# Kernel tuning notes

Hardware: AMD Instinct MI355X
Metric: run time of the kernel (lower is better)

## Reference

```python
import jax, jax.numpy as jnp
import numpy as np

VOL_SIZE = 1.0  # config.render.volume_size


def _make_grid(G, vol_size):
    # pytorch3d Volumes.get_coord_grid(world_coordinates=True): axis-aligned grid
    # centered at origin, spacing = voxel_size = vol_size/G, last dim is (x,y,z)
    # with x varying along W, y along H, z along D.
    m = (G - 1) / 2.0 * (vol_size / G)
    lin = jnp.linspace(-m, m, G, dtype=jnp.float32)
    zz, yy, xx = jnp.meshgrid(lin, lin, lin, indexing='ij')
    return jnp.stack([xx, yy, zz], axis=-1)  # [G,G,G,3]


def _grid_sample_3d(vol, grid):
    # vol: [N,C,D,H,W]; grid: [N,Dg,Hg,Wg,3] xyz in [-1,1].
    # Matches torch F.grid_sample(mode='bilinear', padding_mode='zeros', align_corners=False).
    N, C, D, H, W = vol.shape
    ix = ((grid[..., 0] + 1.0) * W - 1.0) * 0.5
    iy = ((grid[..., 1] + 1.0) * H - 1.0) * 0.5
    iz = ((grid[..., 2] + 1.0) * D - 1.0) * 0.5
    x0f, y0f, z0f = jnp.floor(ix), jnp.floor(iy), jnp.floor(iz)
    tx, ty, tz = ix - x0f, iy - y0f, iz - z0f
    x0, y0, z0 = x0f.astype(jnp.int32), y0f.astype(jnp.int32), z0f.astype(jnp.int32)

    def per_batch(v, z0, y0, x0, tx, ty, tz):
        # v: [C,D,H,W]; index/weight maps: [Dg,Hg,Wg]
        def corner(z, y, x):
            valid = (z >= 0) & (z < D) & (y >= 0) & (y < H) & (x >= 0) & (x < W)
            zc = jnp.clip(z, 0, D - 1)
            yc = jnp.clip(y, 0, H - 1)
            xc = jnp.clip(x, 0, W - 1)
            return v[:, zc, yc, xc] * valid[None]  # [C,Dg,Hg,Wg]
        z1, y1, x1 = z0 + 1, y0 + 1, x0 + 1
        acc = jnp.zeros((C,) + z0.shape, dtype=v.dtype)
        for zc, wz in ((z0, 1.0 - tz), (z1, tz)):
            for yc, wy in ((y0, 1.0 - ty), (y1, ty)):
                for xc, wx in ((x0, 1.0 - tx), (x1, tx)):
                    acc = acc + corner(zc, yc, xc) * (wz * wy * wx)[None]
        return acc

    return jax.vmap(per_batch)(vol, z0, y0, x0, tx, ty, tz)


def reference(voxels, camPoses_cv2, grid_size):
    B, t, C, D, H, W = voxels.shape
    G = grid_size
    m = (G - 1) / 2.0 * (VOL_SIZE / G)  # grid_coord_max
    grid_coord = _make_grid(G, VOL_SIZE)  # [G,G,G,3]

    # T = pose_0 @ pose_1^{-1}, per (B, t-1) pair
    pose0 = jnp.broadcast_to(camPoses_cv2[:, 0:1], (B, t - 1, 4, 4)).reshape(B * (t - 1), 4, 4)
    pose1 = camPoses_cv2[:, 1:].reshape(B * (t - 1), 4, 4)
    T = pose0 @ jnp.linalg.inv(pose1)

    # homogeneous transform of world grid points: cam = R @ p + trans
    pts = grid_coord.reshape(-1, 3)  # [N=G^3, 3]
    R, trans = T[:, :3, :3], T[:, :3, 3]
    cam = jnp.einsum('nij,pj->npi', R, pts) + trans[:, None, :]  # [B*(t-1), N, 3]
    sample_grid = (cam / m).reshape(B * (t - 1), D, H, W, 3)

    warped = _grid_sample_3d(voxels[:, 1:].reshape(B * (t - 1), C, D, H, W), sample_grid)
    out = jnp.concatenate([voxels[:, 0:1], warped.reshape(B, t - 1, C, D, H, W)], axis=1)
    return out


def setup_inputs() -> dict:
    key = jax.random.key(0)
    kv, ka, kt = jax.random.split(key, 3)
    B, t, C, G = 2, 5, 16, 64
    voxels = jax.random.normal(kv, (B, t, C, G, G, G), dtype=jnp.float32)
    # build valid SE(3)-ish camera poses (orthonormal rotation + small translation)
    A = jax.random.normal(ka, (B, t, 3, 3), dtype=jnp.float32)
    Q, _ = jnp.linalg.qr(A)
    det = jnp.linalg.det(Q)
    Q = Q * jnp.sign(det)[..., None, None]  # ensure det=+1
    trans = 0.2 * jax.random.normal(kt, (B, t, 3), dtype=jnp.float32)
    top = jnp.concatenate([Q, trans[..., None]], axis=-1)  # [B,t,3,4]
    bottom = jnp.broadcast_to(jnp.array([0.0, 0.0, 0.0, 1.0], jnp.float32), (B, t, 1, 4))
    camPoses_cv2 = jnp.concatenate([top, bottom], axis=-2)  # [B,t,4,4]
    return {"voxels": voxels, "camPoses_cv2": camPoses_cv2, "grid_size": G}
```

## Files before the change

### kernel.cpp

```cpp
#include <hip/hip_runtime.h>

#define G3_    (64 * 64 * 64)
#define CCH    16
#define TT     5
#define LSTRIDE 17
#define BUF    4096
#define NCHB   4
#define NWARP  (4096 * (CCH / NCHB))
#define NCOPY  8192
#define NBLK   (NWARP + NCOPY)


__global__ void coeff_kernel(const float* __restrict__ cam, float* __restrict__ Tc)
{
    int n = threadIdx.x;
    if (n >= 8) return;
    int b = n >> 2, j = n & 3;
    const float* p0 = cam + (size_t)(b * TT) * 16;
    const float* p1 = cam + (size_t)(b * TT + j + 1) * 16;
    float a00 = p0[0], a01 = p0[1], a02 = p0[2],  at0 = p0[3];
    float a10 = p0[4], a11 = p0[5], a12 = p0[6],  at1 = p0[7];
    float a20 = p0[8], a21 = p0[9], a22 = p0[10], at2 = p0[11];
    float b00 = p1[0], b01 = p1[1], b02 = p1[2],  bt0 = p1[3];
    float b10 = p1[4], b11 = p1[5], b12 = p1[6],  bt1 = p1[7];
    float b20 = p1[8], b21 = p1[9], b22 = p1[10], bt2 = p1[11];
    float R00 = a00*b00 + a01*b01 + a02*b02;
    float R01 = a00*b10 + a01*b11 + a02*b12;
    float R02 = a00*b20 + a01*b21 + a02*b22;
    float R10 = a10*b00 + a11*b01 + a12*b02;
    float R11 = a10*b10 + a11*b11 + a12*b12;
    float R12 = a10*b20 + a11*b21 + a12*b22;
    float R20 = a20*b00 + a21*b01 + a22*b02;
    float R21 = a20*b10 + a21*b11 + a22*b12;
    float R22 = a20*b20 + a21*b21 + a22*b22;
    float trx = at0 - (R00*bt0 + R01*bt1 + R02*bt2);
    float try_= at1 - (R10*bt0 + R11*bt1 + R12*bt2);
    float trz = at2 - (R20*bt0 + R21*bt1 + R22*bt2);

    const float S  = 1.0f / 64.0f;
    const float SC = 32.0f / 0.4921875f;
    float ax = SC * R00 * S, bx = SC * R01 * S, cx = SC * R02 * S;
    float ay = SC * R10 * S, by = SC * R11 * S, cy = SC * R12 * S;
    float az = SC * R20 * S, bz = SC * R21 * S, cz = SC * R22 * S;
    float* o = Tc + n * 12;
    o[0] = ax; o[1] = bx; o[2] = cx;
    o[3] = ay; o[4] = by; o[5] = cy;
    o[6] = az; o[7] = bz; o[8] = cz;
    o[9]  = -31.5f * (ax + bx + cx) + SC * trx + 31.5f;
    o[10] = -31.5f * (ay + by + cy) + SC * try_ + 31.5f;
    o[11] = -31.5f * (az + bz + cz) + SC * trz + 31.5f;
}

__global__ __launch_bounds__(256) void fused_kernel(const float* __restrict__ vox,
                                                    const float* __restrict__ Tc,
                                                    float* __restrict__ out)
{
    __shared__ float lds[BUF];
    const int tid = threadIdx.x;

    const int bid  = blockIdx.x;
    const int sbid = (bid & 7) * (NBLK / 8) + (bid >> 3);
    const int q3   = sbid / 3;
    const int r3   = sbid - q3 * 3;

    if (r3 == 2) {
        int t4 = q3 * 256 + tid;
        int b  = t4 >> 20;
        int rr = t4 & ((1 << 20) - 1);
        size_t base = (size_t)(b * TT) * CCH * G3_;
        const float4* s = (const float4*)(vox + base);
        float4* d = (float4*)(out + base);
        d[rr] = s[rr];
        return;
    }

    const int wid = q3 * 2 + r3;
    const int cg  = wid >> 12;
    const int t9  = wid & 4095;
    const int n   = t9 >> 9;
    const int t6  = t9 & 511;
    const int ox  = (t6 & 7) << 3;
    const int oy  = ((t6 >> 3) & 7) << 3;
    const int oz  = (t6 >> 6) << 3;
    const int b   = n >> 2, j = n & 3;

    const float* Cp = Tc + n * 12;
    const float ax = Cp[0], bx = Cp[1], cx = Cp[2];
    const float ay = Cp[3], by = Cp[4], cy = Cp[5];
    const float az = Cp[6], bz = Cp[7], cz = Cp[8];
    const float kx = Cp[9], ky = Cp[10], kz = Cp[11];

    float x0a = ax * ox, x0b = ax * (ox + 7);
    float x1a = bx * oy, x1b = bx * (oy + 7);
    float x2a = cx * oz, x2b = cx * (oz + 7);
    float min_ix = kx + fminf(x0a, x0b) + fminf(x1a, x1b) + fminf(x2a, x2b);
    float max_ix = kx + fmaxf(x0a, x0b) + fmaxf(x1a, x1b) + fmaxf(x2a, x2b);
    float y0a = ay * ox, y0b = ay * (ox + 7);
    float y1a = by * oy, y1b = by * (oy + 7);
    float y2a = cy * oz, y2b = cy * (oz + 7);
    float min_iy = ky + fminf(y0a, y0b) + fminf(y1a, y1b) + fminf(y2a, y2b);
    float max_iy = ky + fmaxf(y0a, y0b) + fmaxf(y1a, y1b) + fmaxf(y2a, y2b);
    float z0a = az * ox, z0b = az * (ox + 7);
    float z1a = bz * oy, z1b = bz * (oy + 7);
    float z2a = cz * oz, z2b = cz * (oz + 7);
    float min_iz = kz + fminf(z0a, z0b) + fminf(z1a, z1b) + fminf(z2a, z2b);
    float max_iz = kz + fmaxf(z0a, z0b) + fmaxf(z1a, z1b) + fmaxf(z2a, z2b);

    int xlo = min(max((int)floorf(min_ix), 0), 63);
    int xhi = min(max((int)floorf(max_ix) + 1, 0), 63);
    int ylo = min(max((int)floorf(min_iy), 0), 63);
    int yhi = min(max((int)floorf(max_iy) + 1, 0), 63);
    int zlo = min(max((int)floorf(min_iz), 0), 63);
    int zhi = min(max((int)floorf(max_iz) + 1, 0), 63);
    const int xlo_e = xlo & ~1;
    const int sxe = xhi - xlo_e + 1;
    const int sy  = yhi - ylo + 1;
    const int sz  = zhi - zlo + 1;
    const int lstep = sy * LSTRIDE;

    const int gx0 = ox + ((tid & 3) << 1);
    const int gy  = oy + ((tid >> 2) & 7);
    const int gz  = oz + (tid >> 5);
    const float ix0 = kx + ax * gx0 + bx * gy + cx * gz;
    const float iy0 = ky + ay * gx0 + by * gy + cy * gz;
    const float iz0 = kz + az * gx0 + bz * gy + cz * gz;

    float wx0[2], wx1[2], wy0[2], wy1[2], wz0[2], wz1[2];
    int base0[2], base1[2];
    #pragma unroll
    for (int k = 0; k < 2; ++k) {
        float ix = ix0 + (k ? ax : 0.0f);
        float iy = iy0 + (k ? ay : 0.0f);
        float iz = iz0 + (k ? az : 0.0f);
        float fx = floorf(ix), fy = floorf(iy), fz = floorf(iz);
        float tx = ix - fx, ty = iy - fy, tz = iz - fz;
        int X0 = (int)fx, Y0 = (int)fy, Z0 = (int)fz;

        float w0 = ((unsigned)X0 < 64u) ? (1.0f - tx) : 0.0f;
        float w1 = ((unsigned)(X0 + 1) < 64u) ? tx : 0.0f;
        int rxu = X0 - xlo_e;
        wx0[k] = (rxu < 0) ? w1 : w0;
        wx1[k] = (rxu < 0) ? 0.0f : w1;
        int rx0 = min(max(rxu, 0), sxe - 1);

        w0 = ((unsigned)Y0 < 64u) ? (1.0f - ty) : 0.0f;
        w1 = ((unsigned)(Y0 + 1) < 64u) ? ty : 0.0f;
        int ryu = Y0 - ylo;
        wy0[k] = (ryu < 0) ? w1 : w0;
        wy1[k] = (ryu < 0) ? 0.0f : w1;
        int ry0 = min(max(ryu, 0), sy - 1);

        wz0[k] = ((unsigned)Z0 < 64u) ? (1.0f - tz) : 0.0f;
        wz1[k] = ((unsigned)(Z0 + 1) < 64u) ? tz : 0.0f;
        int rz0 = min(max(Z0     - zlo, 0), sz - 1);
        int rz1 = min(max(Z0 + 1 - zlo, 0), sz - 1);

        base0[k] = rz0 * lstep + ry0 * LSTRIDE + rx0;
        base1[k] = rz1 * lstep + ry0 * LSTRIDE + rx0;
    }
    const int soff = (gz << 12) + (gy << 6) + gx0;

    const size_t fb = ((size_t)(b * TT + j + 1) * CCH + cg * NCHB) * G3_;
    const float* vbase = vox + fb;
    float* obase = out + fb;

    const int lane8 = tid & 7;
    const int row16 = (tid >> 3) & 15;
    const int zh    = tid >> 7;
    const int xe    = xlo_e + (lane8 << 1);
    const bool actS = (xe <= xhi) && (row16 < sy);
    const int grow  = (zlo << 12) + ((ylo + row16) << 6) + xe;
    const int lrow  = row16 * LSTRIDE + (lane8 << 1);

    float2 stg[8];

    if (actS) {
        const float2* gp = (const float2*)(vbase + grow);
        #pragma unroll
        for (int k = 0; k < 8; ++k) {
            int zz = (k << 1) + zh;
            if (zz < sz) stg[k] = gp[(size_t)zz << 11];
        }
    }
    #pragma unroll
    for (int i = 0; i < 16; ++i) lds[tid + i * 256] = 0.0f;
    __syncthreads();
    if (actS) {
        #pragma unroll
        for (int k = 0; k < 8; ++k) {
            int zz = (k << 1) + zh;
            if (zz < sz) {
                float* wp = lds + lrow + zz * lstep;
                wp[0] = stg[k].x;
                wp[1] = stg[k].y;
            }
        }
    }
    __syncthreads();

    for (int cc = 0; cc < NCHB; ++cc) {
        const bool pre = (cc + 1 < NCHB);
        if (pre && actS) {
            const float2* gp = (const float2*)(vbase + (size_t)(cc + 1) * G3_ + grow);
            #pragma unroll
            for (int k = 0; k < 8; ++k) {
                int zz = (k << 1) + zh;
                if (zz < sz) stg[k] = gp[(size_t)zz << 11];
            }
        }

        float* op = obase + (size_t)cc * G3_;
        float res[2];
        #pragma unroll
        for (int k = 0; k < 2; ++k) {
            const float* pz0 = lds + base0[k];
            const float* pz1 = lds + base1[k];
            float v000 = pz0[0],  v001 = pz0[1];
            float v010 = pz0[17], v011 = pz0[18];
            float v100 = pz1[0],  v101 = pz1[1];
            float v110 = pz1[17], v111 = pz1[18];
            float t00 = v000 * wx0[k] + v001 * wx1[k];
            float t01 = v010 * wx0[k] + v011 * wx1[k];
            float t10 = v100 * wx0[k] + v101 * wx1[k];
            float t11 = v110 * wx0[k] + v111 * wx1[k];
            float u0  = t00 * wy0[k] + t01 * wy1[k];
            float u1  = t10 * wy0[k] + t11 * wy1[k];
            res[k] = u0 * wz0[k] + u1 * wz1[k];
        }
        *(float2*)(op + soff) = make_float2(res[0], res[1]);

        if (pre) {
            __syncthreads();
            if (actS) {
                #pragma unroll
                for (int k = 0; k < 8; ++k) {
                    int zz = (k << 1) + zh;
                    if (zz < sz) {
                        float* wp = lds + lrow + zz * lstep;
                        wp[0] = stg[k].x;
                        wp[1] = stg[k].y;
                    }
                }
            }
            __syncthreads();
        }
    }
}

extern "C" void kernel_launch(void* const* d_in, const int* in_sizes, int n_in,
                              void* d_out, int out_size, void* d_ws, size_t ws_size,
                              hipStream_t stream)
{
    const float* vox = (const float*)d_in[0];
    const float* cam = (const float*)d_in[1];
    float* out = (float*)d_out;
    float* Tc  = (float*)d_ws;

    hipLaunchKernelGGL(coeff_kernel, dim3(1), dim3(64), 0, stream, cam, Tc);
    hipLaunchKernelGGL(fused_kernel, dim3(NBLK), dim3(256), 0, stream, vox, Tc, out);
}
```

Baseline: 357.5 us.

## Replace LDS-staged brick gather with direct global trilinear gathers per channel

Removes the shared-memory staging of the source bounding box and the 4-channel pipelined loop. Each block now handles one channel and a z-slice of 8 y-rows, and gathers its 8 corners straight from global memory, relying on L2/L1 caching. The copy and warp blocks are interleaved 8:1. This drops the syncs and LDS traffic, but trades them for uncoalesced global gathers and eight global loads per output point.

```diff
diff --git a/kernel.cpp b/kernel.cpp
--- a/kernel.cpp
+++ b/kernel.cpp
@@ -3,10 +3,7 @@
 #define G3_    (64 * 64 * 64)
 #define CCH    16
 #define TT     5
-#define LSTRIDE 17
-#define BUF    4096
-#define NCHB   4
-#define NWARP  (4096 * (CCH / NCHB))
+#define NWARP  65536
 #define NCOPY  8192
 #define NBLK   (NWARP + NCOPY)
 
@@ -55,16 +52,15 @@
                                                     const float* __restrict__ Tc,
                                                     float* __restrict__ out)
 {
-    __shared__ float lds[BUF];
     const int tid = threadIdx.x;
 
     const int bid  = blockIdx.x;
     const int sbid = (bid & 7) * (NBLK / 8) + (bid >> 3);
-    const int q3   = sbid / 3;
-    const int r3   = sbid - q3 * 3;
+    const int q9   = sbid / 9;
+    const int r9   = sbid - q9 * 9;
 
-    if (r3 == 2) {
-        int t4 = q3 * 256 + tid;
+    if (r9 == 8) {
+        int t4 = q9 * 256 + tid;
         int b  = t4 >> 20;
         int rr = t4 & ((1 << 20) - 1);
         size_t base = (size_t)(b * TT) * CCH * G3_;
@@ -74,14 +70,14 @@
         return;
     }
 
-    const int wid = q3 * 2 + r3;
-    const int cg  = wid >> 12;
-    const int t9  = wid & 4095;
-    const int n   = t9 >> 9;
-    const int t6  = t9 & 511;
-    const int ox  = (t6 & 7) << 3;
-    const int oy  = ((t6 >> 3) & 7) << 3;
-    const int oz  = (t6 >> 6) << 3;
+    const int wid = q9 * 8 + r9;
+    const int pc  = wid >> 9;
+    const int rem = wid & 511;
+    const int gz  = rem >> 3;
+    const int gy  = ((rem & 7) << 3) + (tid >> 5);
+    const int gx0 = (tid & 31) << 1;
+    const int n   = pc >> 4;
+    const int c   = pc & 15;
     const int b   = n >> 2, j = n & 3;
 
     const float* Cp = Tc + n * 12;
@@ -90,161 +86,53 @@
     const float az = Cp[6], bz = Cp[7], cz = Cp[8];
     const float kx = Cp[9], ky = Cp[10], kz = Cp[11];
 
-    float x0a = ax * ox, x0b = ax * (ox + 7);
-    float x1a = bx * oy, x1b = bx * (oy + 7);
-    float x2a = cx * oz, x2b = cx * (oz + 7);
-    float min_ix = kx + fminf(x0a, x0b) + fminf(x1a, x1b) + fminf(x2a, x2b);
-    float max_ix = kx + fmaxf(x0a, x0b) + fmaxf(x1a, x1b) + fmaxf(x2a, x2b);
-    float y0a = ay * ox, y0b = ay * (ox + 7);
-    float y1a = by * oy, y1b = by * (oy + 7);
-    float y2a = cy * oz, y2b = cy * (oz + 7);
-    float min_iy = ky + fminf(y0a, y0b) + fminf(y1a, y1b) + fminf(y2a, y2b);
-    float max_iy = ky + fmaxf(y0a, y0b) + fmaxf(y1a, y1b) + fmaxf(y2a, y2b);
-    float z0a = az * ox, z0b = az * (ox + 7);
-    float z1a = bz * oy, z1b = bz * (oy + 7);
-    float z2a = cz * oz, z2b = cz * (oz + 7);
-    float min_iz = kz + fminf(z0a, z0b) + fminf(z1a, z1b) + fminf(z2a, z2b);
-    float max_iz = kz + fmaxf(z0a, z0b) + fmaxf(z1a, z1b) + fmaxf(z2a, z2b);
+    const size_t fb = ((size_t)(b * TT + j + 1) * CCH + c) * G3_;
+    const float* v = vox + fb;
 
-    int xlo = min(max((int)floorf(min_ix), 0), 63);
-    int xhi = min(max((int)floorf(max_ix) + 1, 0), 63);
-    int ylo = min(max((int)floorf(min_iy), 0), 63);
-    int yhi = min(max((int)floorf(max_iy) + 1, 0), 63);
-    int zlo = min(max((int)floorf(min_iz), 0), 63);
-    int zhi = min(max((int)floorf(max_iz) + 1, 0), 63);
-    const int xlo_e = xlo & ~1;
-    const int sxe = xhi - xlo_e + 1;
-    const int sy  = yhi - ylo + 1;
-    const int sz  = zhi - zlo + 1;
-    const int lstep = sy * LSTRIDE;
+    float ix = kx + ax * gx0 + bx * gy + cx * gz;
+    float iy = ky + ay * gx0 + by * gy + cy * gz;
+    float iz = kz + az * gx0 + bz * gy + cz * gz;
 
-    const int gx0 = ox + ((tid & 3) << 1);
-    const int gy  = oy + ((tid >> 2) & 7);
-    const int gz  = oz + (tid >> 5);
-    const float ix0 = kx + ax * gx0 + bx * gy + cx * gz;
-    const float iy0 = ky + ay * gx0 + by * gy + cy * gz;
-    const float iz0 = kz + az * gx0 + bz * gy + cz * gz;
-
-    float wx0[2], wx1[2], wy0[2], wy1[2], wz0[2], wz1[2];
-    int base0[2], base1[2];
+    float res[2];
     #pragma unroll
     for (int k = 0; k < 2; ++k) {
-        float ix = ix0 + (k ? ax : 0.0f);
-        float iy = iy0 + (k ? ay : 0.0f);
-        float iz = iz0 + (k ? az : 0.0f);
+        if (k) { ix += ax; iy += ay; iz += az; }
         float fx = floorf(ix), fy = floorf(iy), fz = floorf(iz);
         float tx = ix - fx, ty = iy - fy, tz = iz - fz;
         int X0 = (int)fx, Y0 = (int)fy, Z0 = (int)fz;
 
-        float w0 = ((unsigned)X0 < 64u) ? (1.0f - tx) : 0.0f;
-        float w1 = ((unsigned)(X0 + 1) < 64u) ? tx : 0.0f;
-        int rxu = X0 - xlo_e;
-        wx0[k] = (rxu < 0) ? w1 : w0;
-        wx1[k] = (rxu < 0) ? 0.0f : w1;
-        int rx0 = min(max(rxu, 0), sxe - 1);
+        float wx0 = ((unsigned)X0       < 64u) ? (1.0f - tx) : 0.0f;
+        float wx1 = ((unsigned)(X0 + 1) < 64u) ? tx          : 0.0f;
+        float wy0 = ((unsigned)Y0       < 64u) ? (1.0f - ty) : 0.0f;
+        float wy1 = ((unsigned)(Y0 + 1) < 64u) ? ty          : 0.0f;
+        float wz0 = ((unsigned)Z0       < 64u) ? (1.0f - tz) : 0.0f;
+        float wz1 = ((unsigned)(Z0 + 1) < 64u) ? tz          : 0.0f;
 
-        w0 = ((unsigned)Y0 < 64u) ? (1.0f - ty) : 0.0f;
-        w1 = ((unsigned)(Y0 + 1) < 64u) ? ty : 0.0f;
-        int ryu = Y0 - ylo;
-        wy0[k] = (ryu < 0) ? w1 : w0;
-        wy1[k] = (ryu < 0) ? 0.0f : w1;
-        int ry0 = min(max(ryu, 0), sy - 1);
+        int xc0 = min(max(X0,     0), 63), xc1 = min(max(X0 + 1, 0), 63);
+        int yc0 = min(max(Y0,     0), 63), yc1 = min(max(Y0 + 1, 0), 63);
+        int zc0 = min(max(Z0,     0), 63), zc1 = min(max(Z0 + 1, 0), 63);
 
-        wz0[k] = ((unsigned)Z0 < 64u) ? (1.0f - tz) : 0.0f;
-        wz1[k] = ((unsigned)(Z0 + 1) < 64u) ? tz : 0.0f;
-        int rz0 = min(max(Z0     - zlo, 0), sz - 1);
-        int rz1 = min(max(Z0 + 1 - zlo, 0), sz - 1);
+        int zy00 = (zc0 << 12) + (yc0 << 6);
+        int zy01 = (zc0 << 12) + (yc1 << 6);
+        int zy10 = (zc1 << 12) + (yc0 << 6);
+        int zy11 = (zc1 << 12) + (yc1 << 6);
 
-        base0[k] = rz0 * lstep + ry0 * LSTRIDE + rx0;
-        base1[k] = rz1 * lstep + ry0 * LSTRIDE + rx0;
+        float v000 = v[zy00 + xc0], v001 = v[zy00 + xc1];
+        float v010 = v[zy01 + xc0], v011 = v[zy01 + xc1];
+        float v100 = v[zy10 + xc0], v101 = v[zy10 + xc1];
+        float v110 = v[zy11 + xc0], v111 = v[zy11 + xc1];
+
+        float t00 = v000 * wx0 + v001 * wx1;
+        float t01 = v010 * wx0 + v011 * wx1;
+        float t10 = v100 * wx0 + v101 * wx1;
+        float t11 = v110 * wx0 + v111 * wx1;
+        float u0  = t00 * wy0 + t01 * wy1;
+        float u1  = t10 * wy0 + t11 * wy1;
+        res[k] = u0 * wz0 + u1 * wz1;
     }
-    const int soff = (gz << 12) + (gy << 6) + gx0;
 
-    const size_t fb = ((size_t)(b * TT + j + 1) * CCH + cg * NCHB) * G3_;
-    const float* vbase = vox + fb;
-    float* obase = out + fb;
-
-    const int lane8 = tid & 7;
-    const int row16 = (tid >> 3) & 15;
-    const int zh    = tid >> 7;
-    const int xe    = xlo_e + (lane8 << 1);
-    const bool actS = (xe <= xhi) && (row16 < sy);
-    const int grow  = (zlo << 12) + ((ylo + row16) << 6) + xe;
-    const int lrow  = row16 * LSTRIDE + (lane8 << 1);
-
-    float2 stg[8];
-
-    if (actS) {
-        const float2* gp = (const float2*)(vbase + grow);
-        #pragma unroll
-        for (int k = 0; k < 8; ++k) {
-            int zz = (k << 1) + zh;
-            if (zz < sz) stg[k] = gp[(size_t)zz << 11];
-        }
-    }
-    #pragma unroll
-    for (int i = 0; i < 16; ++i) lds[tid + i * 256] = 0.0f;
-    __syncthreads();
-    if (actS) {
-        #pragma unroll
-        for (int k = 0; k < 8; ++k) {
-            int zz = (k << 1) + zh;
-            if (zz < sz) {
-                float* wp = lds + lrow + zz * lstep;
-                wp[0] = stg[k].x;
-                wp[1] = stg[k].y;
-            }
-        }
-    }
-    __syncthreads();
-
-    for (int cc = 0; cc < NCHB; ++cc) {
-        const bool pre = (cc + 1 < NCHB);
-        if (pre && actS) {
-            const float2* gp = (const float2*)(vbase + (size_t)(cc + 1) * G3_ + grow);
-            #pragma unroll
-            for (int k = 0; k < 8; ++k) {
-                int zz = (k << 1) + zh;
-                if (zz < sz) stg[k] = gp[(size_t)zz << 11];
-            }
-        }
-
-        float* op = obase + (size_t)cc * G3_;
-        float res[2];
-        #pragma unroll
-        for (int k = 0; k < 2; ++k) {
-            const float* pz0 = lds + base0[k];
-            const float* pz1 = lds + base1[k];
-            float v000 = pz0[0],  v001 = pz0[1];
-            float v010 = pz0[17], v011 = pz0[18];
-            float v100 = pz1[0],  v101 = pz1[1];
-            float v110 = pz1[17], v111 = pz1[18];
-            float t00 = v000 * wx0[k] + v001 * wx1[k];
-            float t01 = v010 * wx0[k] + v011 * wx1[k];
-            float t10 = v100 * wx0[k] + v101 * wx1[k];
-            float t11 = v110 * wx0[k] + v111 * wx1[k];
-            float u0  = t00 * wy0[k] + t01 * wy1[k];
-            float u1  = t10 * wy0[k] + t11 * wy1[k];
-            res[k] = u0 * wz0[k] + u1 * wz1[k];
-        }
-        *(float2*)(op + soff) = make_float2(res[0], res[1]);
-
-        if (pre) {
-            __syncthreads();
-            if (actS) {
-                #pragma unroll
-                for (int k = 0; k < 8; ++k) {
-                    int zz = (k << 1) + zh;
-                    if (zz < sz) {
-                        float* wp = lds + lrow + zz * lstep;
-                        wp[0] = stg[k].x;
-                        wp[1] = stg[k].y;
-                    }
-                }
-            }
-            __syncthreads();
-        }
-    }
+    float* o = out + fb + ((gz << 12) + (gy << 6) + gx0);
+    *(float2*)o = make_float2(res[0], res[1]);
 }
 
 extern "C" void kernel_launch(void* const* d_in, const int* in_sizes, int n_in,
```

Result: slower. 647.8 us (+81.2%).
